# Optimization experiments

Hardware: AMD Instinct MI355X
Metric: run time of the kernel (lower is better)

## Reference

```python
import jax, jax.numpy as jnp
import numpy as np

T, MEM, B, DM, N, D = 1024, 1024, 4, 1024, 16, 64
C = MEM + T
SCALE = 1.0 / D ** 0.5
LN_EPS = 1e-5


def _rel_shift(x):
    # x: [T, C, B, N] -> Transformer-XL relative shift
    t, c = x.shape[0], x.shape[1]
    zero_pad = jnp.zeros((t, 1) + x.shape[2:], x.dtype)
    x_padded = jnp.concatenate([zero_pad, x], axis=1)  # [T, C+1, B, N]
    x_padded = x_padded.reshape((c + 1, t) + x.shape[2:])
    return x_padded[1:].reshape(x.shape)


def setup_inputs() -> dict:
    key = jax.random.key(0)
    ks = jax.random.split(key, 8)
    h = jax.random.normal(ks[0], (T, B, DM), jnp.float32)
    m = jax.random.normal(ks[1], (MEM, B, DM), jnp.float32)
    r = jax.random.normal(ks[2], (C, DM), jnp.float32)
    # causal mask with memory: query i (global pos MEM+i) may attend to j <= MEM+i
    mask = (jnp.arange(C)[None, :] > (jnp.arange(T)[:, None] + MEM))[:, :, None]  # [T,C,1] bool, True=disallow
    W_qkv = jax.random.normal(ks[3], (DM, 3 * N * D), jnp.float32) * 0.02
    W_r = jax.random.normal(ks[4], (DM, N * D), jnp.float32) * 0.02
    W_o = jax.random.normal(ks[5], (N * D, DM), jnp.float32) * 0.02
    r_w_bias = jax.random.normal(ks[6], (N, D), jnp.float32)
    r_r_bias = jax.random.normal(ks[7], (N, D), jnp.float32)
    ln_gamma = jnp.ones((DM,), jnp.float32)
    ln_beta = jnp.zeros((DM,), jnp.float32)
    return {"h": h, "m": m, "r": r, "mask": mask, "W_qkv": W_qkv, "W_r": W_r,
            "W_o": W_o, "r_w_bias": r_w_bias, "r_r_bias": r_r_bias,
            "ln_gamma": ln_gamma, "ln_beta": ln_beta}


def reference(h, m, r, mask, W_qkv, W_r, W_o, r_w_bias, r_r_bias, ln_gamma, ln_beta):
    t, b = h.shape[0], h.shape[1]
    c = r.shape[0]
    cat = jnp.concatenate([m, h], axis=0)          # [C, B, DM]
    w_heads = cat @ W_qkv                           # [C, B, 3*N*D]
    w_q, w_k, w_v = jnp.split(w_heads, 3, axis=-1)
    w_q = w_q[-t:].reshape(t, b, N, D)              # [T,B,N,D]
    w_k = w_k.reshape(c, b, N, D)                   # [C,B,N,D]
    w_v = w_v.reshape(c, b, N, D)                   # [C,B,N,D]
    r_k = (r @ W_r).reshape(c, N, D)                # [C,N,D]
    AC = jnp.einsum('ibnd,jbnd->ijbn', w_q + r_w_bias, w_k)
    BD = jnp.einsum('ibnd,jnd->ijbn', w_q + r_r_bias, r_k)
    BD = _rel_shift(BD)
    score = (AC + BD) * SCALE                       # [T,C,B,N]
    score = jnp.where(mask[:, :, :, None], jnp.float32(-65000.0), score.astype(jnp.float32)).astype(score.dtype)
    prob = jax.nn.softmax(score, axis=1)
    vec = jnp.einsum('ijbn,jbnd->ibnd', prob, w_v).reshape(t, b, N * D)
    attn_out = vec @ W_o                            # [T,B,DM]
    x = h + attn_out
    mu = jnp.mean(x, axis=-1, keepdims=True)
    var = jnp.mean((x - mu) ** 2, axis=-1, keepdims=True)
    return (x - mu) * jax.lax.rsqrt(var + LN_EPS) * ln_gamma + ln_beta
```

## Files before the change

### kernel.cpp

```cpp
#include <hip/hip_runtime.h>
#include <stdint.h>

#define T_LEN 1024
#define MEM_LEN 1024
#define C_LEN 2048
#define B_SZ 4
#define DM_ 1024
#define NH 16
#define HD 64

typedef __attribute__((ext_vector_type(8))) short short8;
typedef __attribute__((ext_vector_type(4))) float f32x4;
typedef __attribute__((ext_vector_type(4))) unsigned short ushort4v;
typedef __attribute__((ext_vector_type(4))) float float4v;

__device__ __forceinline__ unsigned short f2bf(float f) {
  union { float f; unsigned int u; } v; v.f = f;
  unsigned int r = v.u + 0x7fffu + ((v.u >> 16) & 1u);
  return (unsigned short)(r >> 16);
}
__device__ __forceinline__ float bf2f(unsigned short b) {
  union { unsigned int u; float f; } v; v.u = ((unsigned int)b) << 16;
  return v.f;
}
__device__ __forceinline__ f32x4 mfma16(short8 a, short8 b, f32x4 c) {
  return __builtin_amdgcn_mfma_f32_16x16x32_bf16(a, b, c, 0, 0, 0);
}

__global__ void k_cat_convert(const float* __restrict__ m, const float* __restrict__ h,
                              unsigned short* __restrict__ outB) {
  int idx = blockIdx.x * 256 + threadIdx.x;
  const int MQ = (MEM_LEN * B_SZ * DM_) / 4;
  float4v v;
  if (idx < MQ) v = ((const float4v*)m)[idx];
  else          v = ((const float4v*)h)[idx - MQ];
  ushort4v o;
  o.x = f2bf(v.x); o.y = f2bf(v.y); o.z = f2bf(v.z); o.w = f2bf(v.w);
  ((ushort4v*)outB)[idx] = o;
}

__global__ void k_f32_to_bf16(const float* __restrict__ in, unsigned short* __restrict__ outB, int nq) {
  int idx = blockIdx.x * 256 + threadIdx.x;
  if (idx >= nq) return;
  float4v v = ((const float4v*)in)[idx];
  ushort4v o;
  o.x = f2bf(v.x); o.y = f2bf(v.y); o.z = f2bf(v.z); o.w = f2bf(v.w);
  ((ushort4v*)outB)[idx] = o;
}

__global__ void k_transpose_bf16(const float* __restrict__ in, unsigned short* __restrict__ out,
                                 int R, int Ccols) {
  __shared__ float tile[32][33];
  int c0 = blockIdx.x * 32, r0 = blockIdx.y * 32;
  int tx = threadIdx.x & 31, ty = threadIdx.x >> 5;
#pragma unroll
  for (int p = 0; p < 4; ++p)
    tile[ty + 8 * p][tx] = in[(size_t)(r0 + ty + 8 * p) * Ccols + c0 + tx];
  __syncthreads();
#pragma unroll
  for (int p = 0; p < 4; ++p)
    out[(size_t)(c0 + ty + 8 * p) * R + r0 + tx] = f2bf(tile[tx][ty + 8 * p]);
}

template <int MODE>
__global__ __launch_bounds__(256) void k_gemm(const unsigned short* __restrict__ A,
                                              const unsigned short* __restrict__ BT,
                                              void* __restrict__ out1, void* __restrict__ out2,
                                              int M, int N, int K, int ldc) {
  __shared__ unsigned short As[128 * 64];
  __shared__ unsigned short Bs[128 * 64];
  const int tid = threadIdx.x;
  const int w = tid >> 6, l = tid & 63;
  const int wm = w >> 1, wn = w & 1;
  const int lg = l >> 4, lr = l & 15;
  const int gx = gridDim.x;
  const int pid = blockIdx.y * gx + blockIdx.x;
  const int xcd = pid & 7;
  const int idx = pid >> 3;
  const int cb = idx % gx;
  const int rb = (idx / gx) * 8 + xcd;
  const int m0 = rb * 128, n0 = cb * 128;
  f32x4 acc[4][4] = {};
  const int lrow8 = l >> 3;
  const int scol = (l & 7) * 8;
  const unsigned short* Abase = A + (size_t)m0 * K;
  const unsigned short* Bbase = BT + (size_t)n0 * K;
  for (int kt = 0; kt < K; kt += 64) {
    __syncthreads();
#pragma unroll
    for (int q = 0; q < 4; ++q) {
      int chunk = w * 4 + q;
      int row = chunk * 8 + lrow8;
      __builtin_amdgcn_global_load_lds(
          (const __attribute__((address_space(1))) void*)(Abase + (size_t)row * K + kt + scol),
          (__attribute__((address_space(3))) void*)(As + chunk * 512), 16, 0, 0);
      __builtin_amdgcn_global_load_lds(
          (const __attribute__((address_space(1))) void*)(Bbase + (size_t)row * K + kt + scol),
          (__attribute__((address_space(3))) void*)(Bs + chunk * 512), 16, 0, 0);
    }
    __syncthreads();
#pragma unroll
    for (int ks = 0; ks < 2; ++ks) {
      short8 a[4], bb[4];
#pragma unroll
      for (int mi = 0; mi < 4; ++mi)
        a[mi] = *(const short8*)&As[(wm * 64 + mi * 16 + lr) * 64 + ks * 32 + lg * 8];
#pragma unroll
      for (int ni = 0; ni < 4; ++ni)
        bb[ni] = *(const short8*)&Bs[(wn * 64 + ni * 16 + lr) * 64 + ks * 32 + lg * 8];
#pragma unroll
      for (int mi = 0; mi < 4; ++mi)
#pragma unroll
        for (int ni = 0; ni < 4; ++ni)
          acc[mi][ni] = mfma16(a[mi], bb[ni], acc[mi][ni]);
    }
  }
#pragma unroll
  for (int mi = 0; mi < 4; ++mi)
#pragma unroll
    for (int ni = 0; ni < 4; ++ni)
#pragma unroll
      for (int r = 0; r < 4; ++r) {
        int row = m0 + wm * 64 + mi * 16 + lg * 4 + r;
        int cc = n0 + wn * 64 + ni * 16 + lr;
        float val = acc[mi][ni][r];
        if (MODE == 1) {
          ((float*)out1)[(size_t)row * ldc + cc] = val;
        } else if (MODE == 2) {
          int nn = (cc & 1023) >> 6, d = cc & 63;
          int c = row >> 2, b = row & 3;
          size_t addr = ((size_t)((b * 16 + nn) * 2048 + c)) * 64 + d;
          unsigned short* dst = (cc < 1024) ? (unsigned short*)out1 : (unsigned short*)out2;
          dst[addr] = f2bf(val);
        } else if (MODE == 3) {
          int nn = cc >> 6, d = cc & 63;
          int t = row >> 2, b = row & 3;
          ((unsigned short*)out1)[((size_t)((b * 16 + nn) * 1024 + t)) * 64 + d] = f2bf(val);
        } else {
          int nn = cc >> 6, d = cc & 63;
          ((unsigned short*)out1)[((size_t)(nn * 2048 + row)) * 64 + d] = f2bf(val);
        }
      }
}

__global__ void k_vt(const unsigned short* __restrict__ Vp, unsigned short* __restrict__ VT) {
  __shared__ unsigned short tile[64][72];
  int c0 = blockIdx.x * 64;
  int n = blockIdx.y, b = blockIdx.z;
  int t = threadIdx.x;
  const unsigned short* src = Vp + ((size_t)((b * 16 + n) * 2048 + c0)) * 64;
#pragma unroll
  for (int p = 0; p < 16; ++p) {
    int idx = p * 256 + t;
    int r = idx >> 6, d = idx & 63;
    tile[d][r] = src[(size_t)r * 64 + d];
  }
  __syncthreads();
#pragma unroll
  for (int p = 0; p < 16; ++p) {
    int idx = p * 256 + t;
    int d = idx >> 6, c = idx & 63;
    VT[(size_t)((b * 16 + n) * 64 + d) * 2048 + c0 + c] = tile[d][c];
  }
}

__global__ void k_bias_dots(const unsigned short* __restrict__ Kp,
                            const unsigned short* __restrict__ Rkp,
                            const float* __restrict__ rwb, const float* __restrict__ rrb,
                            float* __restrict__ uk, float* __restrict__ vr) {
  int gid = blockIdx.x * 256 + threadIdx.x;
  if (gid < B_SZ * NH * C_LEN) {
    int bn = gid >> 11;
    int n = bn & 15;
    const unsigned short* kp = Kp + (size_t)gid * 64;
    float s = 0.f;
#pragma unroll
    for (int q = 0; q < 8; ++q) {
      short8 v = *(const short8*)&kp[q * 8];
#pragma unroll
      for (int e = 0; e < 8; ++e)
        s += bf2f((unsigned short)v[e]) * rwb[n * 64 + q * 8 + e];
    }
    uk[gid] = s;
  } else {
    int g2 = gid - B_SZ * NH * C_LEN;
    int n = g2 >> 11;
    const unsigned short* rp = Rkp + (size_t)g2 * 64;
    float s = 0.f;
#pragma unroll
    for (int q = 0; q < 8; ++q) {
      short8 v = *(const short8*)&rp[q * 8];
#pragma unroll
      for (int e = 0; e < 8; ++e)
        s += bf2f((unsigned short)v[e]) * rrb[n * 64 + q * 8 + e];
    }
    vr[g2] = s;
  }
}

__device__ __forceinline__ void stage_tile(const unsigned short* __restrict__ Kbase,
                                           const unsigned short* __restrict__ Vbase,
                                           unsigned short* ksBuf, unsigned short* vsBuf,
                                           int j0, int tid) {
#pragma unroll
  for (int q = 0; q < 2; ++q) {
    int chunk = q * 256 + tid;
    int row = chunk >> 3;
    int slot = chunk & 7;
    int ss = slot ^ (row & 7);
    __builtin_amdgcn_global_load_lds(
        (const __attribute__((address_space(1))) void*)(Kbase + (size_t)(j0 + row) * 64 + ss * 8),
        (__attribute__((address_space(3))) void*)(ksBuf + chunk * 8), 16, 0, 0);
    __builtin_amdgcn_global_load_lds(
        (const __attribute__((address_space(1))) void*)(Vbase + (size_t)row * 2048 + j0 + ss * 8),
        (__attribute__((address_space(3))) void*)(vsBuf + chunk * 8), 16, 0, 0);
  }
}

__global__ __launch_bounds__(256) void k_attn(const unsigned short* __restrict__ Qp,
                                              const unsigned short* __restrict__ Kp,
                                              const unsigned short* __restrict__ VT,
                                              const unsigned short* __restrict__ Rkp,
                                              const float* __restrict__ uk,
                                              const float* __restrict__ vr,
                                              unsigned short* __restrict__ po,
                                              float* __restrict__ psumG) {
  __shared__ __align__(16) unsigned short Ks[2][64 * 64];
  __shared__ __align__(16) unsigned short Vs[2][64 * 64];
  __shared__ unsigned short P[4][16][72];
  const int tid = threadIdx.x;
  const int w = tid >> 6, l = tid & 63;
  const int lg = l >> 4, lr = l & 15;
  const int L = blockIdx.x;
  const int bnlo = L & 7;
  const int rest = L >> 3;
  const int bnhi = rest / 48;
  const int inner = rest - bnhi * 48;
  const int xt = inner / 3;
  const int s  = inner - xt * 3;
  const int bn = bnhi * 8 + bnlo;
  const int i0 = xt * 64;
  const int n = bn & 15, b = bn >> 4;
  const int wrow = i0 + w * 16;

  const int ntile = xt + 17;
  const int t0 = (s * ntile) / 3;
  const int t1 = ((s + 1) * ntile) / 3;

  const unsigned short* Kbase = Kp + (size_t)bn * 2048 * 64;
  const unsigned short* Vbase = VT + (size_t)bn * 64 * 2048;
  const unsigned short* Rkbase = Rkp + (size_t)n * 2048 * 64;

  short8 aq0, aq1;
  {
    const unsigned short* qp = Qp + (size_t)(bn * 1024 + wrow + lr) * 64 + lg * 8;
    aq0 = *(const short8*)qp;
    aq1 = *(const short8*)(qp + 32);
  }
  float psum[4];
  f32x4 o[4];
#pragma unroll
  for (int r = 0; r < 4; ++r) psum[r] = 0.f;
#pragma unroll
  for (int df = 0; df < 4; ++df) o[df] = (f32x4){0.f, 0.f, 0.f, 0.f};

  const float* ukp = uk + (size_t)bn * 2048;
  const float* vrp = vr + (size_t)n * 2048;

  stage_tile(Kbase, Vbase, Ks[0], Vs[0], t0 * 64, tid);
  stage_tile(Kbase, Vbase, Ks[1], Vs[1], (t0 + 1) * 64, tid);

  const float EXPC = 0.18033688011112042f;

  for (int jt = t0; jt < t1; ++jt) {
    const int j0 = jt * 64;
    const int cur = (jt - t0) & 1;
    if (jt + 1 < t1) { asm volatile("s_waitcnt vmcnt(4)" ::: "memory"); }
    else             { asm volatile("s_waitcnt vmcnt(0)" ::: "memory"); }
    __builtin_amdgcn_s_barrier();

    f32x4 sac[4];
#pragma unroll
    for (int jf = 0; jf < 4; ++jf) sac[jf] = (f32x4){0.f, 0.f, 0.f, 0.f};
#pragma unroll
    for (int jf = 0; jf < 4; ++jf) {
      int row = jf * 16 + lr;
      int rx = row & 7;
      short8 k0 = *(const short8*)&Ks[cur][row * 64 + ((lg ^ rx) * 8)];
      short8 k1 = *(const short8*)&Ks[cur][row * 64 + (((4 + lg) ^ rx) * 8)];
      sac[jf] = mfma16(aq0, k0, sac[jf]);
      sac[jf] = mfma16(aq1, k1, sac[jf]);
    }
    const int kbw = j0 + 1008 - i0 - w * 16;
    f32x4 gb[5];
#pragma unroll
    for (int jg = 0; jg < 5; ++jg) {
      int rowK = kbw + jg * 16 + lr;
      short8 b0 = {}, b1 = {};
      float vrv = 0.f;
      if (rowK < C_LEN) {
        const unsigned short* rp = Rkbase + (size_t)rowK * 64 + lg * 8;
        b0 = *(const short8*)rp;
        b1 = *(const short8*)(rp + 32);
        vrv = vrp[rowK];
      }
      f32x4 g = (f32x4){0.f, 0.f, 0.f, 0.f};
      g = mfma16(aq0, b0, g);
      g = mfma16(aq1, b1, g);
#pragma unroll
      for (int r = 0; r < 4; ++r) g[r] += vrv;
      gb[jg] = g;
    }
    float ukv[4];
#pragma unroll
    for (int jf = 0; jf < 4; ++jf) ukv[jf] = ukp[j0 + jf * 16 + lr];
    float p[4][4];
#pragma unroll
    for (int r = 0; r < 4; ++r) {
      const int R = lg * 4 + r;
      const int delta = lr + 15 - R;
      const int src = (l & 48) | (delta & 15);
      float v0 = __shfl(gb[0][r], src);
      float v1 = __shfl(gb[1][r], src);
      float v2 = __shfl(gb[2][r], src);
      float v3 = __shfl(gb[3][r], src);
      float v4 = __shfl(gb[4][r], src);
      const bool hi = delta >= 16;
      float bd0 = hi ? v1 : v0;
      float bd1 = hi ? v2 : v1;
      float bd2 = hi ? v3 : v2;
      float bd3 = hi ? v4 : v3;
      const int jlim = i0 + w * 16 + R + MEM_LEN;
      int j = j0 + lr;
      p[0][r] = (j > jlim) ? 0.f : exp2f((sac[0][r] + bd0 + ukv[0]) * EXPC);
      j += 16;
      p[1][r] = (j > jlim) ? 0.f : exp2f((sac[1][r] + bd1 + ukv[1]) * EXPC);
      j += 16;
      p[2][r] = (j > jlim) ? 0.f : exp2f((sac[2][r] + bd2 + ukv[2]) * EXPC);
      j += 16;
      p[3][r] = (j > jlim) ? 0.f : exp2f((sac[3][r] + bd3 + ukv[3]) * EXPC);
    }
#pragma unroll
    for (int jf = 0; jf < 4; ++jf)
#pragma unroll
      for (int r = 0; r < 4; ++r) psum[r] += p[jf][r];
#pragma unroll
    for (int jf = 0; jf < 4; ++jf)
#pragma unroll
      for (int r = 0; r < 4; ++r)
        P[w][lg * 4 + r][jf * 16 + lr] = f2bf(p[jf][r]);
#pragma unroll
    for (int ks = 0; ks < 2; ++ks) {
      short8 ap = *(const short8*)&P[w][lr][ks * 32 + lg * 8];
#pragma unroll
      for (int df = 0; df < 4; ++df) {
        int row = df * 16 + lr;
        int rx = row & 7;
        short8 vv = *(const short8*)&Vs[cur][row * 64 + (((ks * 4 + lg) ^ rx) * 8)];
        o[df] = mfma16(ap, vv, o[df]);
      }
    }
    __builtin_amdgcn_s_barrier();
    if (jt + 2 < t1)
      stage_tile(Kbase, Vbase, Ks[cur], Vs[cur], (jt + 2) * 64, tid);
  }
  const int pbase = (bn * 16 + xt) * 3 + s;
  unsigned short* poB = po + (size_t)pbase * 4096;
#pragma unroll
  for (int r = 0; r < 4; ++r) {
    float v = psum[r];
    v += __shfl_xor(v, 1);
    v += __shfl_xor(v, 2);
    v += __shfl_xor(v, 4);
    v += __shfl_xor(v, 8);
    if (lr == 0) psumG[pbase * 64 + w * 16 + lg * 4 + r] = v;
  }
#pragma unroll
  for (int df = 0; df < 4; ++df)
#pragma unroll
    for (int r = 0; r < 4; ++r)
      poB[(w * 16 + lg * 4 + r) * 64 + df * 16 + lr] = f2bf(o[df][r]);
}

__global__ __launch_bounds__(256) void k_ared(const unsigned short* __restrict__ po,
                                              const float* __restrict__ psumG,
                                              unsigned short* __restrict__ vec) {
  const int idx = blockIdx.x;
  const int tid = threadIdx.x;
  const int bn = idx >> 4, xt = idx & 15;
  const int b = bn >> 4, n = bn & 15;
  __shared__ float rs[64];
  if (tid < 64) {
    const float* q = psumG + idx * 192;
    rs[tid] = q[tid] + q[tid + 64] + q[tid + 128];
  }
  __syncthreads();
  const ushort4v* p0 = (const ushort4v*)(po + (size_t)(idx * 3 + 0) * 4096);
  const ushort4v* p1 = (const ushort4v*)(po + (size_t)(idx * 3 + 1) * 4096);
  const ushort4v* p2 = (const ushort4v*)(po + (size_t)(idx * 3 + 2) * 4096);
#pragma unroll
  for (int k = 0; k < 4; ++k) {
    int e = tid + k * 256;
    int row = e >> 4, d4 = e & 15;
    ushort4v a = p0[e], bb = p1[e], c = p2[e];
    float inv = 1.f / rs[row];
    int t = xt * 64 + row;
    ushort4v ov;
    ov.x = f2bf((bf2f(a.x) + bf2f(bb.x) + bf2f(c.x)) * inv);
    ov.y = f2bf((bf2f(a.y) + bf2f(bb.y) + bf2f(c.y)) * inv);
    ov.z = f2bf((bf2f(a.z) + bf2f(bb.z) + bf2f(c.z)) * inv);
    ov.w = f2bf((bf2f(a.w) + bf2f(bb.w) + bf2f(c.w)) * inv);
    *(ushort4v*)&vec[(size_t)(t * 4 + b) * 1024 + n * 64 + d4 * 4] = ov;
  }
}

__global__ __launch_bounds__(256) void k_ln(const float* __restrict__ xg, const float* __restrict__ h,
                                            const float* __restrict__ gamma, const float* __restrict__ beta,
                                            float* __restrict__ out) {
  const int row = blockIdx.x;
  const int t = threadIdx.x;
  __shared__ float red1[4], red2[4];
  float4v xv = ((const float4v*)(xg + (size_t)row * 1024))[t];
  float4v hv = ((const float4v*)(h + (size_t)row * 1024))[t];
  float x0 = xv.x + hv.x, x1 = xv.y + hv.y, x2 = xv.z + hv.z, x3 = xv.w + hv.w;
  float s = x0 + x1 + x2 + x3;
#pragma unroll
  for (int off = 1; off < 64; off <<= 1) s += __shfl_xor(s, off);
  if ((t & 63) == 0) red1[t >> 6] = s;
  __syncthreads();
  float mean = (red1[0] + red1[1] + red1[2] + red1[3]) * (1.f / 1024.f);
  float d0 = x0 - mean, d1 = x1 - mean, d2 = x2 - mean, d3 = x3 - mean;
  float q = d0 * d0 + d1 * d1 + d2 * d2 + d3 * d3;
#pragma unroll
  for (int off = 1; off < 64; off <<= 1) q += __shfl_xor(q, off);
  if ((t & 63) == 0) red2[t >> 6] = q;
  __syncthreads();
  float var = (red2[0] + red2[1] + red2[2] + red2[3]) * (1.f / 1024.f);
  float rs = rsqrtf(var + 1e-5f);
  float4v gv = ((const float4v*)gamma)[t];
  float4v bv = ((const float4v*)beta)[t];
  float4v ov;
  ov.x = d0 * rs * gv.x + bv.x;
  ov.y = d1 * rs * gv.y + bv.y;
  ov.z = d2 * rs * gv.z + bv.z;
  ov.w = d3 * rs * gv.w + bv.w;
  ((float4v*)(out + (size_t)row * 1024))[t] = ov;
}

extern "C" void kernel_launch(void* const* d_in, const int* in_sizes, int n_in,
                              void* d_out, int out_size, void* d_ws, size_t ws_size,
                              hipStream_t stream) {
  (void)in_sizes; (void)n_in; (void)out_size; (void)ws_size;
  const float* h    = (const float*)d_in[0];
  const float* m    = (const float*)d_in[1];
  const float* r    = (const float*)d_in[2];
  const float* Wqkv = (const float*)d_in[4];
  const float* Wr   = (const float*)d_in[5];
  const float* Wo   = (const float*)d_in[6];
  const float* rwb  = (const float*)d_in[7];
  const float* rrb  = (const float*)d_in[8];
  const float* gam  = (const float*)d_in[9];
  const float* bet  = (const float*)d_in[10];
  float* out = (float*)d_out;

  char* ws = (char*)d_ws;
  unsigned short* catB   = (unsigned short*)(ws + 0);
  unsigned short* WqkvT  = (unsigned short*)(ws + 16777216);
  unsigned short* WrT    = (unsigned short*)(ws + 23068672);
  unsigned short* WoT    = (unsigned short*)(ws + 25165824);
  unsigned short* Vp     = (unsigned short*)(ws + 27262976);
  unsigned short* po     = (unsigned short*)(ws + 44040192);
  unsigned short* VT     = (unsigned short*)(ws + 81788928);
  float* uk              = (float*)(ws + 98566144);
  float* vr              = (float*)(ws + 99090432);
  unsigned short* vec    = (unsigned short*)(ws + 99221504);
  float* xbuf            = (float*)(ws + 107610112);
  unsigned short* rB     = (unsigned short*)(ws + 124387328);
  unsigned short* Kp     = (unsigned short*)(ws + 128581632);
  unsigned short* Qp     = (unsigned short*)(ws + 145358848);
  unsigned short* Rkp    = (unsigned short*)(ws + 153747456);
  float* psumG = (float*)(ws + 124387328);

  hipLaunchKernelGGL(k_cat_convert, dim3(8192), dim3(256), 0, stream, m, h, catB);
  hipLaunchKernelGGL(k_f32_to_bf16, dim3(2048), dim3(256), 0, stream, r, rB, 524288);
  hipLaunchKernelGGL(k_transpose_bf16, dim3(96, 32), dim3(256), 0, stream, Wqkv, WqkvT, 1024, 3072);
  hipLaunchKernelGGL(k_transpose_bf16, dim3(32, 32), dim3(256), 0, stream, Wr, WrT, 1024, 1024);
  hipLaunchKernelGGL(k_transpose_bf16, dim3(32, 32), dim3(256), 0, stream, Wo, WoT, 1024, 1024);
  hipLaunchKernelGGL(k_gemm<2>, dim3(16, 64), dim3(256), 0, stream,
                     catB, WqkvT + (size_t)1024 * 1024, (void*)Kp, (void*)Vp, 8192, 2048, 1024, 0);
  hipLaunchKernelGGL(k_gemm<3>, dim3(8, 32), dim3(256), 0, stream,
                     catB + (size_t)4096 * 1024, WqkvT, (void*)Qp, nullptr, 4096, 1024, 1024, 0);
  hipLaunchKernelGGL(k_gemm<4>, dim3(8, 16), dim3(256), 0, stream,
                     rB, WrT, (void*)Rkp, nullptr, 2048, 1024, 1024, 0);
  hipLaunchKernelGGL(k_vt, dim3(32, 16, 4), dim3(256), 0, stream, Vp, VT);
  hipLaunchKernelGGL(k_bias_dots, dim3(640), dim3(256), 0, stream, Kp, Rkp, rwb, rrb, uk, vr);
  hipLaunchKernelGGL(k_attn, dim3(3072), dim3(256), 0, stream, Qp, Kp, VT, Rkp, uk, vr, po, psumG);
  hipLaunchKernelGGL(k_ared, dim3(1024), dim3(256), 0, stream, po, psumG, vec);
  hipLaunchKernelGGL(k_gemm<1>, dim3(8, 32), dim3(256), 0, stream,
                     vec, WoT, (void*)xbuf, nullptr, 4096, 1024, 1024, 1024);
  hipLaunchKernelGGL(k_ln, dim3(4096), dim3(256), 0, stream, xbuf, h, gam, bet, out);
}
```

Baseline: 345.1 us.

## Widen attention blocks to 128 query rows with 8 waves sharing K/V tiles

The attention kernel now runs 512 threads (8 waves) per block covering 128 query rows instead of 64, so each staged K/V tile in LDS feeds twice as many MFMA rows. Each thread issues one async global-to-LDS load per tile, down from two, and the wait count is adjusted to match. The split-reduction kernel is resized to the new partial layout. It also raises wave priority around the MFMA sections with s_setprio. The trade is fewer, larger blocks, coarser causal tile splitting that may compute more masked work, and possible occupancy limits from the larger block.

```diff
diff --git a/kernel.cpp b/kernel.cpp
--- a/kernel.cpp
+++ b/kernel.cpp
@@ -202,22 +202,18 @@
                                            const unsigned short* __restrict__ Vbase,
                                            unsigned short* ksBuf, unsigned short* vsBuf,
                                            int j0, int tid) {
-#pragma unroll
-  for (int q = 0; q < 2; ++q) {
-    int chunk = q * 256 + tid;
-    int row = chunk >> 3;
-    int slot = chunk & 7;
-    int ss = slot ^ (row & 7);
-    __builtin_amdgcn_global_load_lds(
-        (const __attribute__((address_space(1))) void*)(Kbase + (size_t)(j0 + row) * 64 + ss * 8),
-        (__attribute__((address_space(3))) void*)(ksBuf + chunk * 8), 16, 0, 0);
-    __builtin_amdgcn_global_load_lds(
-        (const __attribute__((address_space(1))) void*)(Vbase + (size_t)row * 2048 + j0 + ss * 8),
-        (__attribute__((address_space(3))) void*)(vsBuf + chunk * 8), 16, 0, 0);
-  }
-}
-
-__global__ __launch_bounds__(256) void k_attn(const unsigned short* __restrict__ Qp,
+  int row = tid >> 3;
+  int slot = tid & 7;
+  int ss = slot ^ (row & 7);
+  __builtin_amdgcn_global_load_lds(
+      (const __attribute__((address_space(1))) void*)(Kbase + (size_t)(j0 + row) * 64 + ss * 8),
+      (__attribute__((address_space(3))) void*)(ksBuf + tid * 8), 16, 0, 0);
+  __builtin_amdgcn_global_load_lds(
+      (const __attribute__((address_space(1))) void*)(Vbase + (size_t)row * 2048 + j0 + ss * 8),
+      (__attribute__((address_space(3))) void*)(vsBuf + tid * 8), 16, 0, 0);
+}
+
+__global__ __launch_bounds__(512) void k_attn(const unsigned short* __restrict__ Qp,
                                               const unsigned short* __restrict__ Kp,
                                               const unsigned short* __restrict__ VT,
                                               const unsigned short* __restrict__ Rkp,
@@ -227,23 +223,23 @@
                                               float* __restrict__ psumG) {
   __shared__ __align__(16) unsigned short Ks[2][64 * 64];
   __shared__ __align__(16) unsigned short Vs[2][64 * 64];
-  __shared__ unsigned short P[4][16][72];
+  __shared__ unsigned short P[8][16][72];
   const int tid = threadIdx.x;
   const int w = tid >> 6, l = tid & 63;
   const int lg = l >> 4, lr = l & 15;
   const int L = blockIdx.x;
   const int bnlo = L & 7;
   const int rest = L >> 3;
-  const int bnhi = rest / 48;
-  const int inner = rest - bnhi * 48;
+  const int bnhi = rest / 24;
+  const int inner = rest - bnhi * 24;
   const int xt = inner / 3;
   const int s  = inner - xt * 3;
   const int bn = bnhi * 8 + bnlo;
-  const int i0 = xt * 64;
+  const int i0 = xt * 128;
   const int n = bn & 15, b = bn >> 4;
   const int wrow = i0 + w * 16;
 
-  const int ntile = xt + 17;
+  const int ntile = 2 * xt + 18;
   const int t0 = (s * ntile) / 3;
   const int t1 = ((s + 1) * ntile) / 3;
 
@@ -275,13 +271,14 @@
   for (int jt = t0; jt < t1; ++jt) {
     const int j0 = jt * 64;
     const int cur = (jt - t0) & 1;
-    if (jt + 1 < t1) { asm volatile("s_waitcnt vmcnt(4)" ::: "memory"); }
+    if (jt + 1 < t1) { asm volatile("s_waitcnt vmcnt(2)" ::: "memory"); }
     else             { asm volatile("s_waitcnt vmcnt(0)" ::: "memory"); }
     __builtin_amdgcn_s_barrier();
 
     f32x4 sac[4];
 #pragma unroll
     for (int jf = 0; jf < 4; ++jf) sac[jf] = (f32x4){0.f, 0.f, 0.f, 0.f};
+    __builtin_amdgcn_s_setprio(1);
 #pragma unroll
     for (int jf = 0; jf < 4; ++jf) {
       int row = jf * 16 + lr;
@@ -291,6 +288,7 @@
       sac[jf] = mfma16(aq0, k0, sac[jf]);
       sac[jf] = mfma16(aq1, k1, sac[jf]);
     }
+    __builtin_amdgcn_s_setprio(0);
     const int kbw = j0 + 1008 - i0 - w * 16;
     f32x4 gb[5];
 #pragma unroll
@@ -349,6 +347,7 @@
 #pragma unroll
       for (int r = 0; r < 4; ++r)
         P[w][lg * 4 + r][jf * 16 + lr] = f2bf(p[jf][r]);
+    __builtin_amdgcn_s_setprio(1);
 #pragma unroll
     for (int ks = 0; ks < 2; ++ks) {
       short8 ap = *(const short8*)&P[w][lr][ks * 32 + lg * 8];
@@ -360,12 +359,13 @@
         o[df] = mfma16(ap, vv, o[df]);
       }
     }
+    __builtin_amdgcn_s_setprio(0);
     __builtin_amdgcn_s_barrier();
     if (jt + 2 < t1)
       stage_tile(Kbase, Vbase, Ks[cur], Vs[cur], (jt + 2) * 64, tid);
   }
-  const int pbase = (bn * 16 + xt) * 3 + s;
-  unsigned short* poB = po + (size_t)pbase * 4096;
+  const int pbase = (bn * 8 + xt) * 3 + s;
+  unsigned short* poB = po + (size_t)pbase * 8192;
 #pragma unroll
   for (int r = 0; r < 4; ++r) {
     float v = psum[r];
@@ -373,7 +373,7 @@
     v += __shfl_xor(v, 2);
     v += __shfl_xor(v, 4);
     v += __shfl_xor(v, 8);
-    if (lr == 0) psumG[pbase * 64 + w * 16 + lg * 4 + r] = v;
+    if (lr == 0) psumG[(size_t)pbase * 128 + w * 16 + lg * 4 + r] = v;
   }
 #pragma unroll
   for (int df = 0; df < 4; ++df)
@@ -387,24 +387,25 @@
                                               unsigned short* __restrict__ vec) {
   const int idx = blockIdx.x;
   const int tid = threadIdx.x;
-  const int bn = idx >> 4, xt = idx & 15;
+  const int bn = idx >> 3, xt = idx & 7;
   const int b = bn >> 4, n = bn & 15;
-  __shared__ float rs[64];
-  if (tid < 64) {
-    const float* q = psumG + idx * 192;
-    rs[tid] = q[tid] + q[tid + 64] + q[tid + 128];
-  }
+  const int base = idx * 3;
+  __shared__ float rs[128];
+  if (tid < 128)
+    rs[tid] = psumG[(size_t)base * 128 + tid] +
+              psumG[(size_t)(base + 1) * 128 + tid] +
+              psumG[(size_t)(base + 2) * 128 + tid];
   __syncthreads();
-  const ushort4v* p0 = (const ushort4v*)(po + (size_t)(idx * 3 + 0) * 4096);
-  const ushort4v* p1 = (const ushort4v*)(po + (size_t)(idx * 3 + 1) * 4096);
-  const ushort4v* p2 = (const ushort4v*)(po + (size_t)(idx * 3 + 2) * 4096);
-#pragma unroll
-  for (int k = 0; k < 4; ++k) {
+  const ushort4v* p0 = (const ushort4v*)(po + (size_t)(base + 0) * 8192);
+  const ushort4v* p1 = (const ushort4v*)(po + (size_t)(base + 1) * 8192);
+  const ushort4v* p2 = (const ushort4v*)(po + (size_t)(base + 2) * 8192);
+#pragma unroll
+  for (int k = 0; k < 8; ++k) {
     int e = tid + k * 256;
     int row = e >> 4, d4 = e & 15;
     ushort4v a = p0[e], bb = p1[e], c = p2[e];
     float inv = 1.f / rs[row];
-    int t = xt * 64 + row;
+    int t = xt * 128 + row;
     ushort4v ov;
     ov.x = f2bf((bf2f(a.x) + bf2f(bb.x) + bf2f(c.x)) * inv);
     ov.y = f2bf((bf2f(a.y) + bf2f(bb.y) + bf2f(c.y)) * inv);
@@ -494,8 +495,8 @@
                      rB, WrT, (void*)Rkp, nullptr, 2048, 1024, 1024, 0);
   hipLaunchKernelGGL(k_vt, dim3(32, 16, 4), dim3(256), 0, stream, Vp, VT);
   hipLaunchKernelGGL(k_bias_dots, dim3(640), dim3(256), 0, stream, Kp, Rkp, rwb, rrb, uk, vr);
-  hipLaunchKernelGGL(k_attn, dim3(3072), dim3(256), 0, stream, Qp, Kp, VT, Rkp, uk, vr, po, psumG);
-  hipLaunchKernelGGL(k_ared, dim3(1024), dim3(256), 0, stream, po, psumG, vec);
+  hipLaunchKernelGGL(k_attn, dim3(1536), dim3(512), 0, stream, Qp, Kp, VT, Rkp, uk, vr, po, psumG);
+  hipLaunchKernelGGL(k_ared, dim3(512), dim3(256), 0, stream, po, psumG, vec);
   hipLaunchKernelGGL(k_gemm<1>, dim3(8, 32), dim3(256), 0, stream,
                      vec, WoT, (void*)xbuf, nullptr, 4096, 1024, 1024, 1024);
   hipLaunchKernelGGL(k_ln, dim3(4096), dim3(256), 0, stream, xbuf, h, gam, bet, out);
```

Result: no change. 351.0 us (+1.7%).

## Fold relative-position biases into query fragments and skip masking on interior tiles

Applied to the files above, without the earlier changes.

Removes the separate bias-dot kernel and its uk/vr buffers. The attention kernel now builds two query fragments, q+r_w_bias for the content term and q+r_r_bias for the position term, and drops the per-tile bias loads and adds. The causal mask is applied only on tiles that can cross the diagonal, and P stores use a packed bf16 convert instruction. This saves a kernel launch, global loads in the inner loop and some ALU work, at the cost of more query registers and rounding q+bias to bf16, which changes precision slightly.

```diff
diff --git a/kernel.cpp b/kernel.cpp
--- a/kernel.cpp
+++ b/kernel.cpp
@@ -22,6 +22,11 @@
 __device__ __forceinline__ float bf2f(unsigned short b) {
   union { unsigned int u; float f; } v; v.u = ((unsigned int)b) << 16;
   return v.f;
+}
+__device__ __forceinline__ unsigned int cvtpk(float lo, float hi) {
+  unsigned int r;
+  asm("v_cvt_pk_bf16_f32 %0, %1, %2" : "=v"(r) : "v"(lo), "v"(hi));
+  return r;
 }
 __device__ __forceinline__ f32x4 mfma16(short8 a, short8 b, f32x4 c) {
   return __builtin_amdgcn_mfma_f32_16x16x32_bf16(a, b, c, 0, 0, 0);
@@ -164,40 +169,6 @@
   }
 }
 
-__global__ void k_bias_dots(const unsigned short* __restrict__ Kp,
-                            const unsigned short* __restrict__ Rkp,
-                            const float* __restrict__ rwb, const float* __restrict__ rrb,
-                            float* __restrict__ uk, float* __restrict__ vr) {
-  int gid = blockIdx.x * 256 + threadIdx.x;
-  if (gid < B_SZ * NH * C_LEN) {
-    int bn = gid >> 11;
-    int n = bn & 15;
-    const unsigned short* kp = Kp + (size_t)gid * 64;
-    float s = 0.f;
-#pragma unroll
-    for (int q = 0; q < 8; ++q) {
-      short8 v = *(const short8*)&kp[q * 8];
-#pragma unroll
-      for (int e = 0; e < 8; ++e)
-        s += bf2f((unsigned short)v[e]) * rwb[n * 64 + q * 8 + e];
-    }
-    uk[gid] = s;
-  } else {
-    int g2 = gid - B_SZ * NH * C_LEN;
-    int n = g2 >> 11;
-    const unsigned short* rp = Rkp + (size_t)g2 * 64;
-    float s = 0.f;
-#pragma unroll
-    for (int q = 0; q < 8; ++q) {
-      short8 v = *(const short8*)&rp[q * 8];
-#pragma unroll
-      for (int e = 0; e < 8; ++e)
-        s += bf2f((unsigned short)v[e]) * rrb[n * 64 + q * 8 + e];
-    }
-    vr[g2] = s;
-  }
-}
-
 __device__ __forceinline__ void stage_tile(const unsigned short* __restrict__ Kbase,
                                            const unsigned short* __restrict__ Vbase,
                                            unsigned short* ksBuf, unsigned short* vsBuf,
@@ -221,8 +192,8 @@
                                               const unsigned short* __restrict__ Kp,
                                               const unsigned short* __restrict__ VT,
                                               const unsigned short* __restrict__ Rkp,
-                                              const float* __restrict__ uk,
-                                              const float* __restrict__ vr,
+                                              const float* __restrict__ rwb,
+                                              const float* __restrict__ rrb,
                                               unsigned short* __restrict__ po,
                                               float* __restrict__ psumG) {
   __shared__ __align__(16) unsigned short Ks[2][64 * 64];
@@ -251,11 +222,22 @@
   const unsigned short* Vbase = VT + (size_t)bn * 64 * 2048;
   const unsigned short* Rkbase = Rkp + (size_t)n * 2048 * 64;
 
-  short8 aq0, aq1;
+  short8 aq0u, aq1u, aq0v, aq1v;
   {
     const unsigned short* qp = Qp + (size_t)(bn * 1024 + wrow + lr) * 64 + lg * 8;
-    aq0 = *(const short8*)qp;
-    aq1 = *(const short8*)(qp + 32);
+    short8 q0 = *(const short8*)qp;
+    short8 q1 = *(const short8*)(qp + 32);
+    const float* up = rwb + n * 64 + lg * 8;
+    const float* vp = rrb + n * 64 + lg * 8;
+#pragma unroll
+    for (int e = 0; e < 8; ++e) {
+      float q0f = bf2f((unsigned short)q0[e]);
+      float q1f = bf2f((unsigned short)q1[e]);
+      aq0u[e] = (short)f2bf(q0f + up[e]);
+      aq1u[e] = (short)f2bf(q1f + up[e + 32]);
+      aq0v[e] = (short)f2bf(q0f + vp[e]);
+      aq1v[e] = (short)f2bf(q1f + vp[e + 32]);
+    }
   }
   float psum[4];
   f32x4 o[4];
@@ -263,9 +245,6 @@
   for (int r = 0; r < 4; ++r) psum[r] = 0.f;
 #pragma unroll
   for (int df = 0; df < 4; ++df) o[df] = (f32x4){0.f, 0.f, 0.f, 0.f};
-
-  const float* ukp = uk + (size_t)bn * 2048;
-  const float* vrp = vr + (size_t)n * 2048;
 
   stage_tile(Kbase, Vbase, Ks[0], Vs[0], t0 * 64, tid);
   stage_tile(Kbase, Vbase, Ks[1], Vs[1], (t0 + 1) * 64, tid);
@@ -288,8 +267,8 @@
       int rx = row & 7;
       short8 k0 = *(const short8*)&Ks[cur][row * 64 + ((lg ^ rx) * 8)];
       short8 k1 = *(const short8*)&Ks[cur][row * 64 + (((4 + lg) ^ rx) * 8)];
-      sac[jf] = mfma16(aq0, k0, sac[jf]);
-      sac[jf] = mfma16(aq1, k1, sac[jf]);
+      sac[jf] = mfma16(aq0u, k0, sac[jf]);
+      sac[jf] = mfma16(aq1u, k1, sac[jf]);
     }
     const int kbw = j0 + 1008 - i0 - w * 16;
     f32x4 gb[5];
@@ -297,23 +276,17 @@
     for (int jg = 0; jg < 5; ++jg) {
       int rowK = kbw + jg * 16 + lr;
       short8 b0 = {}, b1 = {};
-      float vrv = 0.f;
       if (rowK < C_LEN) {
         const unsigned short* rp = Rkbase + (size_t)rowK * 64 + lg * 8;
         b0 = *(const short8*)rp;
         b1 = *(const short8*)(rp + 32);
-        vrv = vrp[rowK];
       }
       f32x4 g = (f32x4){0.f, 0.f, 0.f, 0.f};
-      g = mfma16(aq0, b0, g);
-      g = mfma16(aq1, b1, g);
-#pragma unroll
-      for (int r = 0; r < 4; ++r) g[r] += vrv;
+      g = mfma16(aq0v, b0, g);
+      g = mfma16(aq1v, b1, g);
       gb[jg] = g;
     }
-    float ukv[4];
-#pragma unroll
-    for (int jf = 0; jf < 4; ++jf) ukv[jf] = ukp[j0 + jf * 16 + lr];
+    const bool needMask = (j0 + 63 > i0 + w * 16 + MEM_LEN);
     float p[4][4];
 #pragma unroll
     for (int r = 0; r < 4; ++r) {
@@ -330,25 +303,34 @@
       float bd1 = hi ? v2 : v1;
       float bd2 = hi ? v3 : v2;
       float bd3 = hi ? v4 : v3;
-      const int jlim = i0 + w * 16 + R + MEM_LEN;
-      int j = j0 + lr;
-      p[0][r] = (j > jlim) ? 0.f : exp2f((sac[0][r] + bd0 + ukv[0]) * EXPC);
-      j += 16;
-      p[1][r] = (j > jlim) ? 0.f : exp2f((sac[1][r] + bd1 + ukv[1]) * EXPC);
-      j += 16;
-      p[2][r] = (j > jlim) ? 0.f : exp2f((sac[2][r] + bd2 + ukv[2]) * EXPC);
-      j += 16;
-      p[3][r] = (j > jlim) ? 0.f : exp2f((sac[3][r] + bd3 + ukv[3]) * EXPC);
+      float e0 = exp2f((sac[0][r] + bd0) * EXPC);
+      float e1 = exp2f((sac[1][r] + bd1) * EXPC);
+      float e2 = exp2f((sac[2][r] + bd2) * EXPC);
+      float e3 = exp2f((sac[3][r] + bd3) * EXPC);
+      if (needMask) {
+        const int jlim = i0 + w * 16 + R + MEM_LEN;
+        int j = j0 + lr;
+        e0 = (j > jlim) ? 0.f : e0;  j += 16;
+        e1 = (j > jlim) ? 0.f : e1;  j += 16;
+        e2 = (j > jlim) ? 0.f : e2;  j += 16;
+        e3 = (j > jlim) ? 0.f : e3;
+      }
+      p[0][r] = e0; p[1][r] = e1; p[2][r] = e2; p[3][r] = e3;
     }
 #pragma unroll
     for (int jf = 0; jf < 4; ++jf)
 #pragma unroll
       for (int r = 0; r < 4; ++r) psum[r] += p[jf][r];
 #pragma unroll
-    for (int jf = 0; jf < 4; ++jf)
-#pragma unroll
-      for (int r = 0; r < 4; ++r)
-        P[w][lg * 4 + r][jf * 16 + lr] = f2bf(p[jf][r]);
+    for (int r = 0; r < 4; ++r) {
+      unsigned int a01 = cvtpk(p[0][r], p[1][r]);
+      unsigned int a23 = cvtpk(p[2][r], p[3][r]);
+      const int R = lg * 4 + r;
+      P[w][R][lr]      = (unsigned short)a01;
+      P[w][R][16 + lr] = (unsigned short)(a01 >> 16);
+      P[w][R][32 + lr] = (unsigned short)a23;
+      P[w][R][48 + lr] = (unsigned short)(a23 >> 16);
+    }
 #pragma unroll
     for (int ks = 0; ks < 2; ++ks) {
       short8 ap = *(const short8*)&P[w][lr][ks * 32 + lg * 8];
@@ -471,8 +453,6 @@
   unsigned short* Vp     = (unsigned short*)(ws + 27262976);
   unsigned short* po     = (unsigned short*)(ws + 44040192);
   unsigned short* VT     = (unsigned short*)(ws + 81788928);
-  float* uk              = (float*)(ws + 98566144);
-  float* vr              = (float*)(ws + 99090432);
   unsigned short* vec    = (unsigned short*)(ws + 99221504);
   float* xbuf            = (float*)(ws + 107610112);
   unsigned short* rB     = (unsigned short*)(ws + 124387328);
@@ -493,8 +473,7 @@
   hipLaunchKernelGGL(k_gemm<4>, dim3(8, 16), dim3(256), 0, stream,
                      rB, WrT, (void*)Rkp, nullptr, 2048, 1024, 1024, 0);
   hipLaunchKernelGGL(k_vt, dim3(32, 16, 4), dim3(256), 0, stream, Vp, VT);
-  hipLaunchKernelGGL(k_bias_dots, dim3(640), dim3(256), 0, stream, Kp, Rkp, rwb, rrb, uk, vr);
-  hipLaunchKernelGGL(k_attn, dim3(3072), dim3(256), 0, stream, Qp, Kp, VT, Rkp, uk, vr, po, psumG);
+  hipLaunchKernelGGL(k_attn, dim3(3072), dim3(256), 0, stream, Qp, Kp, VT, Rkp, rwb, rrb, po, psumG);
   hipLaunchKernelGGL(k_ared, dim3(1024), dim3(256), 0, stream, po, psumG, vec);
   hipLaunchKernelGGL(k_gemm<1>, dim3(8, 32), dim3(256), 0, stream,
                      vec, WoT, (void*)xbuf, nullptr, 4096, 1024, 1024, 1024);
```

Measured after the change: 328.0 us. 1.05x faster.
